# Kernel tuning notes

Measured on AMD Instinct MI355X. Metric: run time of the kernel, lower is better.

Reference implementation:

```python
import jax, jax.numpy as jnp
import numpy as np

B, S, F = 128, 256, 40
H, D, NH, L, FF = 64, 128, 4, 2, 2048
REG, BIN, NW = 8, 1, 3
NEG = -1e9


def _ln(x, s, b, eps=1e-5):
    m = x.mean(-1, keepdims=True)
    v = ((x - m) ** 2).mean(-1, keepdims=True)
    return (x - m) / jnp.sqrt(v + eps) * s + b


def setup_inputs() -> dict:
    key = jax.random.key(0)
    ks = list(jax.random.split(key, 40))
    k = iter(ks)
    def rn(shape, s=0.05):
        return jax.random.normal(next(k), shape, jnp.float32) * s
    inp = {}
    inp['x'] = jax.random.normal(next(k), (B, S, F), jnp.float32)
    inp['mask'] = jnp.ones((B, S, F), jnp.float32)
    inp['delta'] = jax.random.uniform(next(k), (B, S, F), jnp.float32)
    # GRU params (torch layout: [3H, in], gates order r,z,n)
    inp['gru_w_ih'] = rn((3 * H, 3 * F))
    inp['gru_w_hh'] = rn((3 * H, H))
    inp['gru_b_ih'] = rn((3 * H,))
    inp['gru_b_hh'] = rn((3 * H,))
    inp['dm_w'] = rn((D, H)); inp['dm_b'] = rn((D,))
    # transformer layers stacked on leading dim L
    inp['in_proj_w'] = rn((L, 3 * D, D)); inp['in_proj_b'] = rn((L, 3 * D))
    inp['out_proj_w'] = rn((L, D, D)); inp['out_proj_b'] = rn((L, D))
    inp['lin1_w'] = rn((L, FF, D)); inp['lin1_b'] = rn((L, FF))
    inp['lin2_w'] = rn((L, D, FF)); inp['lin2_b'] = rn((L, D))
    inp['ln1_s'] = jnp.ones((L, D), jnp.float32); inp['ln1_b'] = jnp.zeros((L, D), jnp.float32)
    inp['ln2_s'] = jnp.ones((L, D), jnp.float32); inp['ln2_b'] = jnp.zeros((L, D), jnp.float32)
    inp['score_w'] = rn((1, D)); inp['score_b'] = rn((1,))
    inp['reg_w'] = rn((NW, REG, D)); inp['reg_b'] = rn((NW, REG))
    inp['bin_w'] = rn((NW, BIN, D)); inp['bin_b'] = rn((NW, BIN))
    inp['window_id'] = jax.random.randint(next(k), (B,), 0, NW, jnp.int32)
    return inp


def reference(x, mask, delta, gru_w_ih, gru_w_hh, gru_b_ih, gru_b_hh, dm_w, dm_b,
              in_proj_w, in_proj_b, out_proj_w, out_proj_b, lin1_w, lin1_b,
              lin2_w, lin2_b, ln1_s, ln1_b, ln2_s, ln2_b, score_w, score_b,
              reg_w, reg_b, bin_w, bin_b, window_id):
    inp = jnp.concatenate([x, mask, delta], -1)          # [B,S,3F]
    xw = inp @ gru_w_ih.T + gru_b_ih                      # [B,S,3H] precomputed input gates

    def step(h, xw_t):
        gh = h @ gru_w_hh.T + gru_b_hh
        xr, xz, xn = jnp.split(xw_t, 3, -1)
        hr, hz, hn = jnp.split(gh, 3, -1)
        r = jax.nn.sigmoid(xr + hr)
        zg = jax.nn.sigmoid(xz + hz)
        n = jnp.tanh(xn + r * hn)
        h_new = (1.0 - zg) * n + zg * h
        return h_new, h_new

    h0 = jnp.zeros((x.shape[0], H), x.dtype)
    _, hs = jax.lax.scan(step, h0, jnp.swapaxes(xw, 0, 1))  # [S,B,H]
    z = jnp.swapaxes(hs, 0, 1) @ dm_w.T + dm_b              # [B,S,D]

    time_mask = mask.sum(-1) > 0                            # [B,S] bool
    bias = jnp.where(time_mask[:, None, None, :], 0.0, NEG).astype(z.dtype)
    dh = D // NH
    scale = 1.0 / np.sqrt(dh)

    for l in range(L):  # post-LN torch TransformerEncoderLayer
        qkv = z @ in_proj_w[l].T + in_proj_b[l]
        q, k, v = jnp.split(qkv, 3, -1)
        q = q.reshape(B, S, NH, dh).transpose(0, 2, 1, 3)
        k = k.reshape(B, S, NH, dh).transpose(0, 2, 1, 3)
        v = v.reshape(B, S, NH, dh).transpose(0, 2, 1, 3)
        attn = jax.nn.softmax(jnp.einsum('bhqd,bhkd->bhqk', q, k) * scale + bias, -1)
        o = jnp.einsum('bhqk,bhkd->bhqd', attn, v).transpose(0, 2, 1, 3).reshape(B, S, D)
        z = _ln(z + (o @ out_proj_w[l].T + out_proj_b[l]), ln1_s[l], ln1_b[l])
        ff = jax.nn.relu(z @ lin1_w[l].T + lin1_b[l]) @ lin2_w[l].T + lin2_b[l]
        z = _ln(z + ff, ln2_s[l], ln2_b[l])

    scores = (z @ score_w.T + score_b)[..., 0]              # [B,S]
    scores = jnp.where(time_mask, scores, NEG)
    alpha = jax.nn.softmax(scores, 1)
    pooled = jnp.einsum('bsd,bs->bd', z, alpha)             # [B,D]

    # routed heads: gather 1-of-3 head weights per sample, batched matvec
    y_reg = jnp.einsum('bod,bd->bo', reg_w[window_id], pooled) + reg_b[window_id]
    y_bin = jnp.einsum('bod,bd->bo', bin_w[window_id], pooled) + bin_b[window_id]
    return (y_reg, y_bin)
```

## Files before the change

kernel.cpp:

```cpp
#include <hip/hip_runtime.h>

typedef __attribute__((ext_vector_type(8))) short short8;
typedef __attribute__((ext_vector_type(4))) float f32x4;
typedef unsigned short u16;

#define BB   128
#define SS   256
#define FIN  40
#define HH   64
#define DD   128
#define NHH  4
#define LL   2
#define NEGV (-1e9f)

__device__ __forceinline__ u16 f2b(float f) {
    unsigned u = __float_as_uint(f);
    return (u16)((u + 0x7FFFu + ((u >> 16) & 1u)) >> 16);
}
__device__ __forceinline__ float b2f(u16 u) {
    return __uint_as_float(((unsigned)u) << 16);
}

__global__ __launch_bounds__(256) void cvt_all_kernel(const float* __restrict__ dm_w,
                                                      const float* __restrict__ ip_w,
                                                      const float* __restrict__ op_w,
                                                      const float* __restrict__ l1_w,
                                                      const float* __restrict__ l2_w,
                                                      u16* __restrict__ o_dm, u16* __restrict__ o_ip,
                                                      u16* __restrict__ o_op, u16* __restrict__ o_l1,
                                                      u16* __restrict__ o_l2) {
    int blk = blockIdx.x;
    const float* s; u16* d; int off;
    if      (blk < 4)   { s = dm_w; d = o_dm; off = blk; }
    else if (blk < 52)  { s = ip_w; d = o_ip; off = blk - 4; }
    else if (blk < 68)  { s = op_w; d = o_op; off = blk - 52; }
    else if (blk < 324) { s = l1_w; d = o_l1; off = blk - 68; }
    else                { s = l2_w; d = o_l2; off = blk - 324; }
    int i = (off * 256 + threadIdx.x) * 8;
    float4 a = *(const float4*)&s[i];
    float4 b = *(const float4*)&s[i + 4];
    short8 o;
    o[0] = (short)f2b(a.x); o[1] = (short)f2b(a.y); o[2] = (short)f2b(a.z); o[3] = (short)f2b(a.w);
    o[4] = (short)f2b(b.x); o[5] = (short)f2b(b.y); o[6] = (short)f2b(b.z); o[7] = (short)f2b(b.w);
    *(short8*)&d[i] = o;
}

__global__ __launch_bounds__(256) void tm_kernel(const float* __restrict__ mask,
                                                 float* __restrict__ tm) {
    int i = blockIdx.x * blockDim.x + threadIdx.x;
    if (i >= BB * SS) return;
    const float* m = mask + (size_t)i * FIN;
    float s = 0.f;
    for (int f = 0; f < FIN; ++f) s += m[f];
    tm[i] = (s > 0.f) ? 1.f : 0.f;
}

__global__ __launch_bounds__(192) void xw_kernel(const float* __restrict__ x,
                                                 const float* __restrict__ mask,
                                                 const float* __restrict__ delta,
                                                 const float* __restrict__ w_ih,
                                                 const float* __restrict__ b_ih,
                                                 float* __restrict__ xwt) {
    __shared__ float inp[16][120];
    __shared__ float wl[192][21];
    int group = blockIdx.x >> 8;
    int t = blockIdx.x & 255;
    int tid = threadIdx.x;

    for (int idx = tid; idx < 16 * 120; idx += 192) {
        int r = idx / 120, k = idx % 120;
        size_t g = (size_t)(group * 16 + r) * 256 + t;
        float v;
        if (k < 40)      v = x[g * FIN + k];
        else if (k < 80) v = mask[g * FIN + (k - 40)];
        else             v = delta[g * FIN + (k - 80)];
        inp[r][k] = v;
    }

    float acc[16];
#pragma unroll
    for (int r = 0; r < 16; ++r) acc[r] = 0.f;

    for (int kt = 0; kt < 6; ++kt) {
        __syncthreads();
        for (int idx = tid; idx < 192 * 20; idx += 192) {
            int r = idx / 20, k = idx % 20;
            wl[r][k] = w_ih[(size_t)r * 120 + kt * 20 + k];
        }
        __syncthreads();
#pragma unroll
        for (int kk = 0; kk < 20; ++kk) {
            float w = wl[tid][kk];
            int kg = kt * 20 + kk;
#pragma unroll
            for (int r = 0; r < 16; ++r) acc[r] += w * inp[r][kg];
        }
    }
    float bias = b_ih[tid];
    float* o = xwt + ((size_t)(group * 256 + t) * 192 + tid) * 16;
#pragma unroll
    for (int r = 0; r < 16; r += 4) {
        float4 v = {acc[r] + bias, acc[r + 1] + bias, acc[r + 2] + bias, acc[r + 3] + bias};
        *(float4*)&o[r] = v;
    }
}

__device__ __forceinline__ float gru_gate(float xr, float xz, float xn,
                                          float ar, float az, float an, float hold) {
    float r  = 1.f / (1.f + __expf(-(xr + ar)));
    float zg = 1.f / (1.f + __expf(-(xz + az)));
    float nx = xn + r * an;
    float n  = 2.f / (1.f + __expf(-2.f * nx)) - 1.f;
    return (1.f - zg) * n + zg * hold;
}

__global__ __launch_bounds__(512, 1) void gru_scan_kernel(const float* __restrict__ w_hh,
                                                          const float* __restrict__ b_hh,
                                                          const float* __restrict__ xwt,
                                                          u16* __restrict__ hsb) {
    __shared__ __align__(16) u16 hb[2][16 * 64];
    __shared__ __align__(16) u16 hstage[8][16 * 64];
    int b0 = blockIdx.x * 16;
    int tid = threadIdx.x;
    int w = tid >> 6, lane = tid & 63;
    int fr = lane & 15, hi = lane >> 4;
    int cw = w & 3;
    int jg = w >> 2;

    for (int idx = tid; idx < 1024; idx += 512) hb[0][idx] = 0;

    int c = cw * 16 + fr;
    float br_ = b_hh[c], bz_ = b_hh[64 + c], bn_ = b_hh[128 + c];

    short8 wfr[2], wfz[2], wfn[2];
#pragma unroll
    for (int ks = 0; ks < 2; ++ks) {
        int slot = ks * 4 + hi;
        const float* p0 = w_hh + (size_t)c * 64 + slot * 8;
        const float* p1 = w_hh + (size_t)(64 + c) * 64 + slot * 8;
        const float* p2 = w_hh + (size_t)(128 + c) * 64 + slot * 8;
#pragma unroll
        for (int q = 0; q < 8; ++q) {
            wfr[ks][q] = (short)f2b(p0[q]);
            wfz[ks][q] = (short)f2b(p1[q]);
            wfn[ks][q] = (short)f2b(p2[q]);
        }
    }

    const float* xg = xwt + (size_t)blockIdx.x * (256 * 192 * 16);
    int lo = hi * 4 + jg * 2;

    float hrA = 0.f, hrB = 0.f;

    int woA = (lo + 0) * 64 + ((((c >> 3) ^ ((lo + 0) & 7))) << 3) + (c & 7);
    int woB = (lo + 1) * 64 + ((((c >> 3) ^ ((lo + 1) & 7))) << 3) + (c & 7);
    int soA = (lo + 0) * 64 + c;
    int soB = (lo + 1) * 64 + c;

    float2 pxr[4], pxz[4], pxn[4];
#pragma unroll
    for (int u = 0; u < 4; ++u) {
        pxr[u] = *(const float2*)&xg[((size_t)u * 192 + c) * 16 + lo];
        pxz[u] = *(const float2*)&xg[((size_t)u * 192 + 64 + c) * 16 + lo];
        pxn[u] = *(const float2*)&xg[((size_t)u * 192 + 128 + c) * 16 + lo];
    }
    __syncthreads();

    int cur = 0;
    auto step = [&](float2 xr2, float2 xz2, float2 xn2, int ts) {
        f32x4 ar = {br_, br_, br_, br_};
        f32x4 az = {bz_, bz_, bz_, bz_};
        f32x4 an = {bn_, bn_, bn_, bn_};
#pragma unroll
        for (int ks = 0; ks < 2; ++ks) {
            int soff = (((ks << 2) + hi) ^ (fr & 7)) << 3;
            short8 af = *(const short8*)&hb[cur][fr * 64 + soff];
            ar = __builtin_amdgcn_mfma_f32_16x16x32_bf16(af, wfr[ks], ar, 0, 0, 0);
            az = __builtin_amdgcn_mfma_f32_16x16x32_bf16(af, wfz[ks], az, 0, 0, 0);
            an = __builtin_amdgcn_mfma_f32_16x16x32_bf16(af, wfn[ks], an, 0, 0, 0);
        }
        float aR0, aR1, aZ0, aZ1, aN0, aN1;
        if (jg == 0) { aR0 = ar[0]; aR1 = ar[1]; aZ0 = az[0]; aZ1 = az[1]; aN0 = an[0]; aN1 = an[1]; }
        else         { aR0 = ar[2]; aR1 = ar[3]; aZ0 = az[2]; aZ1 = az[3]; aN0 = an[2]; aN1 = an[3]; }
        hrA = gru_gate(xr2.x, xz2.x, xn2.x, aR0, aZ0, aN0, hrA);
        hrB = gru_gate(xr2.y, xz2.y, xn2.y, aR1, aZ1, aN1, hrB);
        u16 v0 = f2b(hrA), v1 = f2b(hrB);
        int nxt = cur ^ 1;
        hb[nxt][woA] = v0; hb[nxt][woB] = v1;
        hstage[ts][soA] = v0; hstage[ts][soB] = v1;
        asm volatile("s_waitcnt lgkmcnt(0)\n\ts_barrier" ::: "memory");
        cur = nxt;
    };

    for (int t = 0; t < SS; t += 8) {
#pragma unroll
        for (int u = 0; u < 8; ++u) {
            int tp = t + u + 4; tp = (tp < SS) ? tp : (SS - 1);
            float2 nr = *(const float2*)&xg[((size_t)tp * 192 + c) * 16 + lo];
            float2 nz = *(const float2*)&xg[((size_t)tp * 192 + 64 + c) * 16 + lo];
            float2 nn = *(const float2*)&xg[((size_t)tp * 192 + 128 + c) * 16 + lo];
            step(pxr[u & 3], pxz[u & 3], pxn[u & 3], u);
            pxr[u & 3] = nr; pxz[u & 3] = nz; pxn[u & 3] = nn;
        }
#pragma unroll
        for (int f = 0; f < 2; ++f) {
            int idx = tid + f * 512;
            int c8 = idx & 7, pair = idx >> 3;
            int ts = pair >> 4, row = pair & 15;
            short8 v = *(const short8*)&hstage[ts][row * 64 + c8 * 8];
            *(short8*)&hsb[((size_t)(b0 + row) * SS + t + ts) * 64 + c8 * 8] = v;
        }
        asm volatile("s_waitcnt lgkmcnt(0)\n\ts_barrier" ::: "memory");
    }
}

__device__ __forceinline__ void gl_lds16(const void* g, void* s) {
    __builtin_amdgcn_global_load_lds(
        (const __attribute__((address_space(1))) void*)g,
        (__attribute__((address_space(3))) void*)s, 16, 0, 0);
}

template <int MODE, bool RELU>
__global__ __launch_bounds__(256, 2) void mfma_gemm(const u16* __restrict__ A,
                                                    const u16* __restrict__ W,
                                                    const float* __restrict__ bias,
                                                    float* __restrict__ C,
                                                    u16* __restrict__ Cb,
                                                    const float* __restrict__ lns,
                                                    const float* __restrict__ lnb,
                                                    int M, int N, int K) {
    __shared__ __align__(16) u16 Al[128 * 64];
    __shared__ __align__(16) u16 Bl[128 * 64];
    __shared__ float lred[2][2][128];
    int bm = blockIdx.x, bn = blockIdx.y;
    int tid = threadIdx.x;
    int w = tid >> 6, lane = tid & 63;
    int wrow = (w >> 1) * 64, wcol = (w & 1) * 64;
    int fr = lane & 15, hi = lane >> 4;
    int rl = lane >> 3;
    int sl = lane & 7;
    int ssl = sl ^ rl;

    const u16* Ag = A + ((size_t)bm * 128) * K + ssl * 8;
    const u16* Wg = W + ((size_t)bn * 128) * K + ssl * 8;

    f32x4 acc[4][4];
#pragma unroll
    for (int i = 0; i < 4; ++i)
#pragma unroll
        for (int jj = 0; jj < 4; ++jj) acc[i][jj] = (f32x4){0.f, 0.f, 0.f, 0.f};

    int ar[4], br[4];
#pragma unroll
    for (int m = 0; m < 4; ++m) {
        ar[m] = (wrow + m * 16 + fr) * 64;
        br[m] = (wcol + m * 16 + fr) * 64;
    }
    int swz = (fr & 7);

    for (int kt = 0; kt < K; kt += 64) {
        __syncthreads();
#pragma unroll
        for (int i = 0; i < 4; ++i) {
            int c = w * 4 + i;
            int row = c * 8 + rl;
            gl_lds16(Ag + (size_t)row * K + kt, &Al[c * 512]);
            gl_lds16(Wg + (size_t)row * K + kt, &Bl[c * 512]);
        }
        __syncthreads();
#pragma unroll
        for (int kk = 0; kk < 2; ++kk) {
            short8 a[4], bq[4];
            int soff = (((kk << 2) + hi) ^ swz) << 3;
#pragma unroll
            for (int m = 0; m < 4; ++m)
                a[m] = *(const short8*)&Al[ar[m] + soff];
#pragma unroll
            for (int n = 0; n < 4; ++n)
                bq[n] = *(const short8*)&Bl[br[n] + soff];
#pragma unroll
            for (int m = 0; m < 4; ++m)
#pragma unroll
                for (int n = 0; n < 4; ++n)
                    acc[m][n] = __builtin_amdgcn_mfma_f32_16x16x32_bf16(a[m], bq[n], acc[m][n], 0, 0, 0);
        }
    }

    float bv[4];
#pragma unroll
    for (int n = 0; n < 4; ++n) bv[n] = bias[bn * 128 + wcol + n * 16 + fr];

    if (MODE == 4) {
        float v[4][4][4];
#pragma unroll
        for (int m = 0; m < 4; ++m)
#pragma unroll
            for (int j = 0; j < 4; ++j) {
                int row = bm * 128 + wrow + m * 16 + hi * 4 + j;
#pragma unroll
                for (int n = 0; n < 4; ++n)
                    v[m][n][j] = acc[m][n][j] + bv[n] + C[(size_t)row * 128 + wcol + n * 16 + fr];
            }
#pragma unroll
        for (int m = 0; m < 4; ++m)
#pragma unroll
            for (int j = 0; j < 4; ++j) {
                float s = v[m][0][j] + v[m][1][j] + v[m][2][j] + v[m][3][j];
                float q = v[m][0][j]*v[m][0][j] + v[m][1][j]*v[m][1][j]
                        + v[m][2][j]*v[m][2][j] + v[m][3][j]*v[m][3][j];
#pragma unroll
                for (int off = 1; off <= 8; off <<= 1) {
                    s += __shfl_xor(s, off);
                    q += __shfl_xor(q, off);
                }
                if (fr == 0) {
                    int lrow = wrow + m * 16 + hi * 4 + j;
                    lred[0][w & 1][lrow] = s;
                    lred[1][w & 1][lrow] = q;
                }
            }
        __syncthreads();
        float sv[4], bb[4];
#pragma unroll
        for (int n = 0; n < 4; ++n) {
            sv[n] = lns[wcol + n * 16 + fr];
            bb[n] = lnb[wcol + n * 16 + fr];
        }
#pragma unroll
        for (int m = 0; m < 4; ++m)
#pragma unroll
            for (int j = 0; j < 4; ++j) {
                int lrow = wrow + m * 16 + hi * 4 + j;
                float mean = (lred[0][0][lrow] + lred[0][1][lrow]) * (1.f / 128.f);
                float msq  = (lred[1][0][lrow] + lred[1][1][lrow]) * (1.f / 128.f);
                float rstd = rsqrtf(msq - mean * mean + 1e-5f);
                int row = bm * 128 + lrow;
#pragma unroll
                for (int n = 0; n < 4; ++n) {
                    int col = wcol + n * 16 + fr;
                    float o = (v[m][n][j] - mean) * rstd * sv[n] + bb[n];
                    C[(size_t)row * 128 + col] = o;
                    Cb[(size_t)row * 128 + col] = f2b(o);
                }
            }
    } else {
#pragma unroll
        for (int m = 0; m < 4; ++m) {
#pragma unroll
            for (int j = 0; j < 4; ++j) {
                int row = bm * 128 + wrow + m * 16 + hi * 4 + j;
#pragma unroll
                for (int n = 0; n < 4; ++n) {
                    int col = bn * 128 + wcol + n * 16 + fr;
                    float vv = acc[m][n][j] + bv[n];
                    if (RELU) vv = fmaxf(vv, 0.f);
                    if (MODE & 1) C[(size_t)row * N + col] = vv;
                    if (MODE & 2) Cb[(size_t)row * N + col] = f2b(vv);
                }
            }
        }
    }
}

__global__ __launch_bounds__(256, 1) void ff_fused_kernel(const u16* __restrict__ zbin,
                                                          const u16* __restrict__ w1,
                                                          const float* __restrict__ b1,
                                                          const u16* __restrict__ w2,
                                                          const float* __restrict__ b2,
                                                          const float* __restrict__ lns,
                                                          const float* __restrict__ lnb,
                                                          float* __restrict__ z,
                                                          u16* __restrict__ zbout) {
    __shared__ __align__(16) u16 ZB[2][128 * 64];
    __shared__ __align__(16) u16 W1C[2][128 * 64];
    __shared__ __align__(16) u16 W2C[2][128 * 64];
    __shared__ __align__(16) u16 A1[2][128 * 64];
    __shared__ float lred[2][2][128];
    int bm = blockIdx.x;
    int tid = threadIdx.x;
    int w = tid >> 6, lane = tid & 63;
    int wrow = (w >> 1) * 64, wcol = (w & 1) * 64;
    int fr = lane & 15, hi = lane >> 4;
    int rl = lane >> 3, ssl = (lane & 7) ^ rl;
    int swz = fr & 7;
    int xh = wrow >> 6;

#pragma unroll
    for (int hk = 0; hk < 2; ++hk)
#pragma unroll
        for (int i = 0; i < 4; ++i) {
            int ch = w * 4 + i, row = ch * 8 + rl;
            gl_lds16(zbin + ((size_t)(bm * 128 + row)) * 128 + hk * 64 + ssl * 8, &ZB[hk][ch * 512]);
        }

    f32x4 acc2[4][4];
#pragma unroll
    for (int m = 0; m < 4; ++m)
#pragma unroll
        for (int n = 0; n < 4; ++n) acc2[m][n] = (f32x4){0.f, 0.f, 0.f, 0.f};

    for (int ci = 0; ci < 16; ++ci) {
#pragma unroll
        for (int hk = 0; hk < 2; ++hk)
#pragma unroll
            for (int i = 0; i < 4; ++i) {
                int ch = w * 4 + i, row = ch * 8 + rl;
                gl_lds16(w1 + ((size_t)(ci * 128 + row)) * 128 + hk * 64 + ssl * 8, &W1C[hk][ch * 512]);
                gl_lds16(w2 + ((size_t)row) * 2048 + ci * 128 + hk * 64 + ssl * 8, &W2C[hk][ch * 512]);
            }
        __syncthreads();

        f32x4 acc1[4][4];
#pragma unroll
        for (int m = 0; m < 4; ++m)
#pragma unroll
            for (int n = 0; n < 4; ++n) acc1[m][n] = (f32x4){0.f, 0.f, 0.f, 0.f};
#pragma unroll
        for (int ks = 0; ks < 4; ++ks) {
            int hk = ks >> 1;
            int soff = ((((ks & 1) << 2) + hi) ^ swz) << 3;
            short8 a[4], b[4];
#pragma unroll
            for (int m = 0; m < 4; ++m)
                a[m] = *(const short8*)&W1C[hk][(wrow + m * 16 + fr) * 64 + soff];
#pragma unroll
            for (int n = 0; n < 4; ++n)
                b[n] = *(const short8*)&ZB[hk][(wcol + n * 16 + fr) * 64 + soff];
#pragma unroll
            for (int m = 0; m < 4; ++m)
#pragma unroll
                for (int n = 0; n < 4; ++n)
                    acc1[m][n] = __builtin_amdgcn_mfma_f32_16x16x32_bf16(a[m], b[n], acc1[m][n], 0, 0, 0);
        }
#pragma unroll
        for (int m = 0; m < 4; ++m) {
            int x0 = wrow + m * 16 + hi * 4;
            float4 bb = *(const float4*)&b1[ci * 128 + x0];
            int slot = (x0 & 63) >> 3;
            int wadd = x0 & 7;
#pragma unroll
            for (int n = 0; n < 4; ++n) {
                int r = wcol + n * 16 + fr;
                float v0 = fmaxf(acc1[m][n][0] + bb.x, 0.f);
                float v1 = fmaxf(acc1[m][n][1] + bb.y, 0.f);
                float v2 = fmaxf(acc1[m][n][2] + bb.z, 0.f);
                float v3 = fmaxf(acc1[m][n][3] + bb.w, 0.f);
                uint2 pk;
                pk.x = (unsigned)f2b(v0) | ((unsigned)f2b(v1) << 16);
                pk.y = (unsigned)f2b(v2) | ((unsigned)f2b(v3) << 16);
                *(uint2*)&A1[xh][r * 64 + ((slot ^ (r & 7)) << 3) + wadd] = pk;
            }
        }
        __syncthreads();

#pragma unroll
        for (int ks = 0; ks < 4; ++ks) {
            int hk = ks >> 1;
            int soff = ((((ks & 1) << 2) + hi) ^ swz) << 3;
            short8 a[4], b[4];
#pragma unroll
            for (int m = 0; m < 4; ++m)
                a[m] = *(const short8*)&W2C[hk][(wrow + m * 16 + fr) * 64 + soff];
#pragma unroll
            for (int n = 0; n < 4; ++n)
                b[n] = *(const short8*)&A1[hk][(wcol + n * 16 + fr) * 64 + soff];
#pragma unroll
            for (int m = 0; m < 4; ++m)
#pragma unroll
                for (int n = 0; n < 4; ++n)
                    acc2[m][n] = __builtin_amdgcn_mfma_f32_16x16x32_bf16(a[m], b[n], acc2[m][n], 0, 0, 0);
        }
        __syncthreads();
    }

    float vv[4][4][4];
#pragma unroll
    for (int m = 0; m < 4; ++m) {
        int x0 = wrow + m * 16 + hi * 4;
        float4 bb = *(const float4*)&b2[x0];
#pragma unroll
        for (int n = 0; n < 4; ++n) {
            int y = wcol + n * 16 + fr;
            float4 zo = *(const float4*)&z[((size_t)(bm * 128 + y)) * 128 + x0];
            vv[m][n][0] = acc2[m][n][0] + bb.x + zo.x;
            vv[m][n][1] = acc2[m][n][1] + bb.y + zo.y;
            vv[m][n][2] = acc2[m][n][2] + bb.z + zo.z;
            vv[m][n][3] = acc2[m][n][3] + bb.w + zo.w;
        }
    }
#pragma unroll
    for (int n = 0; n < 4; ++n) {
        float s = 0.f, q = 0.f;
#pragma unroll
        for (int m = 0; m < 4; ++m)
#pragma unroll
            for (int j = 0; j < 4; ++j) { float v = vv[m][n][j]; s += v; q += v * v; }
        s += __shfl_xor(s, 16); s += __shfl_xor(s, 32);
        q += __shfl_xor(q, 16); q += __shfl_xor(q, 32);
        if (hi == 0) {
            int y = wcol + n * 16 + fr;
            lred[0][xh][y] = s;
            lred[1][xh][y] = q;
        }
    }
    __syncthreads();
#pragma unroll
    for (int n = 0; n < 4; ++n) {
        int y = wcol + n * 16 + fr;
        float mean = (lred[0][0][y] + lred[0][1][y]) * (1.f / 128.f);
        float msq  = (lred[1][0][y] + lred[1][1][y]) * (1.f / 128.f);
        float rstd = rsqrtf(msq - mean * mean + 1e-5f);
#pragma unroll
        for (int m = 0; m < 4; ++m) {
            int x0 = wrow + m * 16 + hi * 4;
            float4 sv = *(const float4*)&lns[x0];
            float4 bv = *(const float4*)&lnb[x0];
            float o0 = (vv[m][n][0] - mean) * rstd * sv.x + bv.x;
            float o1 = (vv[m][n][1] - mean) * rstd * sv.y + bv.y;
            float o2 = (vv[m][n][2] - mean) * rstd * sv.z + bv.z;
            float o3 = (vv[m][n][3] - mean) * rstd * sv.w + bv.w;
            size_t zoff = ((size_t)(bm * 128 + y)) * 128 + x0;
            *(float4*)&z[zoff] = (float4){o0, o1, o2, o3};
            uint2 pk;
            pk.x = (unsigned)f2b(o0) | ((unsigned)f2b(o1) << 16);
            pk.y = (unsigned)f2b(o2) | ((unsigned)f2b(o3) << 16);
            *(uint2*)&zbout[zoff] = pk;
        }
    }
}

__global__ __launch_bounds__(256) void attn_mfma_kernel(const u16* __restrict__ qkv,
                                                        const float* __restrict__ tm,
                                                        u16* __restrict__ attno) {
    __shared__ __align__(16) u16 Kl[256 * 40];
    __shared__ __align__(16) u16 Vt[32 * 264];
    __shared__ __align__(16) u16 Pl[4][64 * 72];
    __shared__ float tmb[256];
    int bh = blockIdx.x;
    int b = bh >> 2, hd = bh & 3;
    int tid = threadIdx.x;
    int w = tid >> 6, lane = tid & 63;
    int fr = lane & 15, hi = lane >> 4;
    const u16* base = qkv + (size_t)b * SS * 384 + hd * 32;

    for (int idx = tid; idx < 1024; idx += 256) {
        int r = idx >> 2, s = idx & 3;
        short8 v = *(const short8*)(base + (size_t)r * 384 + 128 + s * 8);
        *(short8*)&Kl[r * 40 + s * 8] = v;
    }
    for (int idx = tid; idx < 1024; idx += 256) {
        int r = idx >> 2, s = idx & 3;
        short8 v = *(const short8*)(base + (size_t)r * 384 + 256 + s * 8);
#pragma unroll
        for (int q = 0; q < 8; ++q) Vt[(s * 8 + q) * 264 + r] = (u16)v[q];
    }
    tmb[tid] = (tm[b * SS + tid] > 0.f) ? 0.f : NEGV;

    int q0 = w * 64;
    short8 qf[4];
#pragma unroll
    for (int m = 0; m < 4; ++m)
        qf[m] = *(const short8*)(base + (size_t)(q0 + m * 16 + fr) * 384 + hi * 8);
    __syncthreads();

    const float scale = 0.17677669529663687f;
    f32x4 accO[4][2];
#pragma unroll
    for (int m = 0; m < 4; ++m) {
        accO[m][0] = (f32x4){0.f, 0.f, 0.f, 0.f};
        accO[m][1] = (f32x4){0.f, 0.f, 0.f, 0.f};
    }
    float den[4][4];
#pragma unroll
    for (int m = 0; m < 4; ++m)
#pragma unroll
        for (int j = 0; j < 4; ++j) den[m][j] = 0.f;

    u16* pw = &Pl[w][0];

    for (int kt = 0; kt < 4; ++kt) {
        f32x4 accS[4][4];
#pragma unroll
        for (int m = 0; m < 4; ++m)
#pragma unroll
            for (int n = 0; n < 4; ++n) accS[m][n] = (f32x4){0.f, 0.f, 0.f, 0.f};
        short8 kf[4];
#pragma unroll
        for (int n = 0; n < 4; ++n)
            kf[n] = *(const short8*)&Kl[(kt * 64 + n * 16 + fr) * 40 + hi * 8];
#pragma unroll
        for (int m = 0; m < 4; ++m)
#pragma unroll
            for (int n = 0; n < 4; ++n)
                accS[m][n] = __builtin_amdgcn_mfma_f32_16x16x32_bf16(qf[m], kf[n], accS[m][n], 0, 0, 0);

        float bias[4];
#pragma unroll
        for (int n = 0; n < 4; ++n) bias[n] = tmb[kt * 64 + n * 16 + fr];

#pragma unroll
        for (int m = 0; m < 4; ++m) {
            float rs0 = 0.f, rs1 = 0.f, rs2 = 0.f, rs3 = 0.f;
#pragma unroll
            for (int n = 0; n < 4; ++n) {
                float p0 = __expf(accS[m][n][0] * scale + bias[n]);
                float p1 = __expf(accS[m][n][1] * scale + bias[n]);
                float p2 = __expf(accS[m][n][2] * scale + bias[n]);
                float p3 = __expf(accS[m][n][3] * scale + bias[n]);
                rs0 += p0; rs1 += p1; rs2 += p2; rs3 += p3;
                int cb = n * 16 + fr;
                pw[(m * 16 + hi * 4 + 0) * 72 + cb] = f2b(p0);
                pw[(m * 16 + hi * 4 + 1) * 72 + cb] = f2b(p1);
                pw[(m * 16 + hi * 4 + 2) * 72 + cb] = f2b(p2);
                pw[(m * 16 + hi * 4 + 3) * 72 + cb] = f2b(p3);
            }
#pragma unroll
            for (int off = 1; off <= 8; off <<= 1) {
                rs0 += __shfl_xor(rs0, off);
                rs1 += __shfl_xor(rs1, off);
                rs2 += __shfl_xor(rs2, off);
                rs3 += __shfl_xor(rs3, off);
            }
            den[m][0] += rs0; den[m][1] += rs1; den[m][2] += rs2; den[m][3] += rs3;
        }
        asm volatile("s_waitcnt lgkmcnt(0)" ::: "memory");

#pragma unroll
        for (int ks = 0; ks < 2; ++ks) {
            short8 pf[4], vf[2];
#pragma unroll
            for (int m = 0; m < 4; ++m)
                pf[m] = *(const short8*)&pw[(m * 16 + fr) * 72 + ks * 32 + hi * 8];
#pragma unroll
            for (int nd = 0; nd < 2; ++nd)
                vf[nd] = *(const short8*)&Vt[(nd * 16 + fr) * 264 + kt * 64 + ks * 32 + hi * 8];
#pragma unroll
            for (int m = 0; m < 4; ++m)
#pragma unroll
                for (int nd = 0; nd < 2; ++nd)
                    accO[m][nd] = __builtin_amdgcn_mfma_f32_16x16x32_bf16(pf[m], vf[nd], accO[m][nd], 0, 0, 0);
        }
    }

    u16* orow = attno + (size_t)(b * SS + q0) * DD + hd * 32;
#pragma unroll
    for (int m = 0; m < 4; ++m)
#pragma unroll
        for (int j = 0; j < 4; ++j) {
            float inv = 1.f / den[m][j];
            int qr = m * 16 + hi * 4 + j;
            orow[(size_t)qr * DD + fr]      = f2b(accO[m][0][j] * inv);
            orow[(size_t)qr * DD + 16 + fr] = f2b(accO[m][1][j] * inv);
        }
}

__global__ __launch_bounds__(256) void pool_all_kernel(const float* __restrict__ z,
                                                       const float* __restrict__ score_w,
                                                       const float* __restrict__ score_b,
                                                       const float* __restrict__ tm,
                                                       const float* __restrict__ reg_w,
                                                       const float* __restrict__ reg_b,
                                                       const float* __restrict__ bin_w,
                                                       const float* __restrict__ bin_b,
                                                       const int* __restrict__ wid,
                                                       float* __restrict__ out) {
    int b = blockIdx.x;
    int tid = threadIdx.x;
    __shared__ float sw[128];
    __shared__ float al[SS];
    __shared__ float red[8];
    __shared__ float pp[2][128];
    __shared__ float p[128];

    if (tid < 128) sw[tid] = score_w[tid];
    __syncthreads();

    const float* zr = z + ((size_t)b * SS + tid) * DD;
    float acc = 0.f;
#pragma unroll
    for (int j = 0; j < 128; j += 4) {
        float4 a = *(const float4*)&zr[j];
        float4 wv = *(const float4*)&sw[j];
        acc += a.x * wv.x + a.y * wv.y + a.z * wv.z + a.w * wv.w;
    }
    float sc = acc + score_b[0];
    sc = (tm[b * SS + tid] > 0.f) ? sc : NEGV;

    float m = sc;
#pragma unroll
    for (int off = 32; off; off >>= 1) m = fmaxf(m, __shfl_xor(m, off));
    if ((tid & 63) == 0) red[tid >> 6] = m;
    __syncthreads();
    m = fmaxf(fmaxf(red[0], red[1]), fmaxf(red[2], red[3]));
    float e = __expf(sc - m);
    float ssum = e;
#pragma unroll
    for (int off = 32; off; off >>= 1) ssum += __shfl_xor(ssum, off);
    if ((tid & 63) == 0) red[4 + (tid >> 6)] = ssum;
    __syncthreads();
    ssum = red[4] + red[5] + red[6] + red[7];
    al[tid] = e / ssum;
    __syncthreads();

    int d = tid & 127, half = tid >> 7;
    float pa = 0.f;
    for (int t = half; t < SS; t += 2) pa += al[t] * z[((size_t)b * SS + t) * DD + d];
    pp[half][d] = pa;
    __syncthreads();
    if (tid < 128) p[tid] = pp[0][tid] + pp[1][tid];
    __syncthreads();

    if (tid < 9) {
        int wi = wid[b];
        const float* wrow;
        float bias;
        if (tid < 8) { wrow = reg_w + ((size_t)wi * 8 + tid) * 128; bias = reg_b[wi * 8 + tid]; }
        else         { wrow = bin_w + (size_t)wi * 128;             bias = bin_b[wi]; }
        float hacc = bias;
        for (int k = 0; k < 128; ++k) hacc += wrow[k] * p[k];
        if (tid < 8) out[b * 8 + tid] = hacc;
        else         out[1024 + b] = hacc;
    }
}

extern "C" void kernel_launch(void* const* d_in, const int* in_sizes, int n_in,
                              void* d_out, int out_size, void* d_ws, size_t ws_size,
                              hipStream_t stream) {
    const float* x         = (const float*)d_in[0];
    const float* mask      = (const float*)d_in[1];
    const float* delta     = (const float*)d_in[2];
    const float* gru_w_ih  = (const float*)d_in[3];
    const float* gru_w_hh  = (const float*)d_in[4];
    const float* gru_b_ih  = (const float*)d_in[5];
    const float* gru_b_hh  = (const float*)d_in[6];
    const float* dm_w      = (const float*)d_in[7];
    const float* dm_b      = (const float*)d_in[8];
    const float* in_proj_w = (const float*)d_in[9];
    const float* in_proj_b = (const float*)d_in[10];
    const float* out_proj_w= (const float*)d_in[11];
    const float* out_proj_b= (const float*)d_in[12];
    const float* lin1_w    = (const float*)d_in[13];
    const float* lin1_b    = (const float*)d_in[14];
    const float* lin2_w    = (const float*)d_in[15];
    const float* lin2_b    = (const float*)d_in[16];
    const float* ln1_s     = (const float*)d_in[17];
    const float* ln1_bb    = (const float*)d_in[18];
    const float* ln2_s     = (const float*)d_in[19];
    const float* ln2_bb    = (const float*)d_in[20];
    const float* score_w   = (const float*)d_in[21];
    const float* score_b   = (const float*)d_in[22];
    const float* reg_w     = (const float*)d_in[23];
    const float* reg_b     = (const float*)d_in[24];
    const float* bin_w     = (const float*)d_in[25];
    const float* bin_b     = (const float*)d_in[26];
    const int*   window_id = (const int*)d_in[27];
    float* out = (float*)d_out;

    char* w8 = (char*)d_ws;
    float* z      = (float*)(w8 + 0);
    u16*   zb     = (u16*)  (w8 + 16777216);
    u16*   hsb    = (u16*)  (w8 + 25165824);
    u16*   wb_dm  = (u16*)  (w8 + 29360128);
    u16*   wb_ip  = (u16*)  (w8 + 29376512);
    u16*   wb_op  = (u16*)  (w8 + 29573120);
    u16*   wb_l1  = (u16*)  (w8 + 29638656);
    u16*   wb_l2  = (u16*)  (w8 + 30687232);
    float* tm     = (float*)(w8 + 31735808);
    float* xwt    = (float*)(w8 + 32063488);
    u16*   qkvb   = (u16*)  (w8 + 32063488);
    u16*   attnob = (u16*)  (w8 + 57229312);

    cvt_all_kernel<<<580, 256, 0, stream>>>(dm_w, in_proj_w, out_proj_w, lin1_w, lin2_w,
                                            wb_dm, wb_ip, wb_op, wb_l1, wb_l2);

    tm_kernel<<<(BB * SS + 255) / 256, 256, 0, stream>>>(mask, tm);
    xw_kernel<<<2048, 192, 0, stream>>>(x, mask, delta, gru_w_ih, gru_b_ih, xwt);
    gru_scan_kernel<<<8, 512, 0, stream>>>(gru_w_hh, gru_b_hh, xwt, hsb);

    mfma_gemm<3, false><<<dim3(256, 1), 256, 0, stream>>>(
        hsb, wb_dm, dm_b, z, zb, nullptr, nullptr, 32768, 128, 64);

    for (int l = 0; l < LL; ++l) {
        mfma_gemm<2, false><<<dim3(256, 3), 256, 0, stream>>>(
            zb, wb_ip + (size_t)l * 49152, in_proj_b + l * 384, nullptr, qkvb,
            nullptr, nullptr, 32768, 384, 128);
        attn_mfma_kernel<<<BB * NHH, 256, 0, stream>>>(qkvb, tm, attnob);
        mfma_gemm<4, false><<<dim3(256, 1), 256, 0, stream>>>(
            attnob, wb_op + (size_t)l * 16384, out_proj_b + l * 128, z, zb,
            ln1_s + l * 128, ln1_bb + l * 128, 32768, 128, 128);
        ff_fused_kernel<<<256, 256, 0, stream>>>(
            zb, wb_l1 + (size_t)l * 262144, lin1_b + l * 2048,
            wb_l2 + (size_t)l * 262144, lin2_b + l * 128,
            ln2_s + l * 128, ln2_bb + l * 128, z, zb);
    }

    pool_all_kernel<<<BB, 256, 0, stream>>>(z, score_w, score_b, tm,
                                            reg_w, reg_b, bin_w, bin_b, window_id, out);
}
```

Baseline: 503.0 us.

## Stage GRU input gates into LDS via async double-buffered global_load_lds

```diff
diff --git a/kernel.cpp b/kernel.cpp
--- a/kernel.cpp
+++ b/kernel.cpp
@@ -19,6 +19,12 @@
 }
 __device__ __forceinline__ float b2f(u16 u) {
     return __uint_as_float(((unsigned)u) << 16);
+}
+
+__device__ __forceinline__ void gl_lds16(const void* g, void* s) {
+    __builtin_amdgcn_global_load_lds(
+        (const __attribute__((address_space(1))) void*)g,
+        (__attribute__((address_space(3))) void*)s, 16, 0, 0);
 }
 
 __global__ __launch_bounds__(256) void cvt_all_kernel(const float* __restrict__ dm_w,
@@ -118,8 +124,9 @@
                                                           const float* __restrict__ b_hh,
                                                           const float* __restrict__ xwt,
                                                           u16* __restrict__ hsb) {
+    __shared__ __align__(16) float xbuf[2][4 * 3072];
     __shared__ __align__(16) u16 hb[2][16 * 64];
-    __shared__ __align__(16) u16 hstage[8][16 * 64];
+    __shared__ __align__(16) u16 hstage[4][16 * 64];
     int b0 = blockIdx.x * 16;
     int tid = threadIdx.x;
     int w = tid >> 6, lane = tid & 63;
@@ -147,7 +154,7 @@
         }
     }
 
-    const float* xg = xwt + (size_t)blockIdx.x * (256 * 192 * 16);
+    const char* xgb = (const char*)(xwt + (size_t)blockIdx.x * (256 * 192 * 16));
     int lo = hi * 4 + jg * 2;
 
     float hrA = 0.f, hrB = 0.f;
@@ -157,67 +164,61 @@
     int soA = (lo + 0) * 64 + c;
     int soB = (lo + 1) * 64 + c;
 
-    float2 pxr[4], pxz[4], pxn[4];
-#pragma unroll
-    for (int u = 0; u < 4; ++u) {
-        pxr[u] = *(const float2*)&xg[((size_t)u * 192 + c) * 16 + lo];
-        pxz[u] = *(const float2*)&xg[((size_t)u * 192 + 64 + c) * 16 + lo];
-        pxn[u] = *(const float2*)&xg[((size_t)u * 192 + 128 + c) * 16 + lo];
-    }
+    auto stage = [&](int g, int buf) {
+#pragma unroll
+        for (int i = 0; i < 6; ++i) {
+            int ch = w * 6 + i;
+            gl_lds16(xgb + (size_t)g * 49152 + ch * 1024 + lane * 16,
+                     (char*)&xbuf[buf][0] + ch * 1024 + lane * 16);
+        }
+    };
+
+    stage(0, 0);
+    asm volatile("s_waitcnt vmcnt(0)" ::: "memory");
     __syncthreads();
 
-    int cur = 0;
-    auto step = [&](float2 xr2, float2 xz2, float2 xn2, int ts) {
-        f32x4 ar = {br_, br_, br_, br_};
-        f32x4 az = {bz_, bz_, bz_, bz_};
-        f32x4 an = {bn_, bn_, bn_, bn_};
-#pragma unroll
-        for (int ks = 0; ks < 2; ++ks) {
-            int soff = (((ks << 2) + hi) ^ (fr & 7)) << 3;
-            short8 af = *(const short8*)&hb[cur][fr * 64 + soff];
-            ar = __builtin_amdgcn_mfma_f32_16x16x32_bf16(af, wfr[ks], ar, 0, 0, 0);
-            az = __builtin_amdgcn_mfma_f32_16x16x32_bf16(af, wfz[ks], az, 0, 0, 0);
-            an = __builtin_amdgcn_mfma_f32_16x16x32_bf16(af, wfn[ks], an, 0, 0, 0);
-        }
-        float aR0, aR1, aZ0, aZ1, aN0, aN1;
-        if (jg == 0) { aR0 = ar[0]; aR1 = ar[1]; aZ0 = az[0]; aZ1 = az[1]; aN0 = an[0]; aN1 = an[1]; }
-        else         { aR0 = ar[2]; aR1 = ar[3]; aZ0 = az[2]; aZ1 = az[3]; aN0 = an[2]; aN1 = an[3]; }
-        hrA = gru_gate(xr2.x, xz2.x, xn2.x, aR0, aZ0, aN0, hrA);
-        hrB = gru_gate(xr2.y, xz2.y, xn2.y, aR1, aZ1, aN1, hrB);
-        u16 v0 = f2b(hrA), v1 = f2b(hrB);
-        int nxt = cur ^ 1;
-        hb[nxt][woA] = v0; hb[nxt][woB] = v1;
-        hstage[ts][soA] = v0; hstage[ts][soB] = v1;
-        asm volatile("s_waitcnt lgkmcnt(0)\n\ts_barrier" ::: "memory");
-        cur = nxt;
-    };
-
-    for (int t = 0; t < SS; t += 8) {
-#pragma unroll
-        for (int u = 0; u < 8; ++u) {
-            int tp = t + u + 4; tp = (tp < SS) ? tp : (SS - 1);
-            float2 nr = *(const float2*)&xg[((size_t)tp * 192 + c) * 16 + lo];
-            float2 nz = *(const float2*)&xg[((size_t)tp * 192 + 64 + c) * 16 + lo];
-            float2 nn = *(const float2*)&xg[((size_t)tp * 192 + 128 + c) * 16 + lo];
-            step(pxr[u & 3], pxz[u & 3], pxn[u & 3], u);
-            pxr[u & 3] = nr; pxz[u & 3] = nz; pxn[u & 3] = nn;
-        }
-#pragma unroll
-        for (int f = 0; f < 2; ++f) {
-            int idx = tid + f * 512;
-            int c8 = idx & 7, pair = idx >> 3;
+    int cur = 0, buf = 0;
+    for (int g = 0; g < 64; ++g) {
+        if (g + 1 < 64) stage(g + 1, buf ^ 1);
+#pragma unroll
+        for (int ts = 0; ts < 4; ++ts) {
+            const float* xs = &xbuf[buf][ts * 3072];
+            float2 xr2 = *(const float2*)&xs[c * 16 + lo];
+            float2 xz2 = *(const float2*)&xs[(64 + c) * 16 + lo];
+            float2 xn2 = *(const float2*)&xs[(128 + c) * 16 + lo];
+
+            f32x4 ar = {br_, br_, br_, br_};
+            f32x4 az = {bz_, bz_, bz_, bz_};
+            f32x4 an = {bn_, bn_, bn_, bn_};
+#pragma unroll
+            for (int ks = 0; ks < 2; ++ks) {
+                int soff = (((ks << 2) + hi) ^ (fr & 7)) << 3;
+                short8 af = *(const short8*)&hb[cur][fr * 64 + soff];
+                ar = __builtin_amdgcn_mfma_f32_16x16x32_bf16(af, wfr[ks], ar, 0, 0, 0);
+                az = __builtin_amdgcn_mfma_f32_16x16x32_bf16(af, wfz[ks], az, 0, 0, 0);
+                an = __builtin_amdgcn_mfma_f32_16x16x32_bf16(af, wfn[ks], an, 0, 0, 0);
+            }
+            float aR0, aR1, aZ0, aZ1, aN0, aN1;
+            if (jg == 0) { aR0 = ar[0]; aR1 = ar[1]; aZ0 = az[0]; aZ1 = az[1]; aN0 = an[0]; aN1 = an[1]; }
+            else         { aR0 = ar[2]; aR1 = ar[3]; aZ0 = az[2]; aZ1 = az[3]; aN0 = an[2]; aN1 = an[3]; }
+            hrA = gru_gate(xr2.x, xz2.x, xn2.x, aR0, aZ0, aN0, hrA);
+            hrB = gru_gate(xr2.y, xz2.y, xn2.y, aR1, aZ1, aN1, hrB);
+            u16 v0 = f2b(hrA), v1 = f2b(hrB);
+            int nxt = cur ^ 1;
+            hb[nxt][woA] = v0; hb[nxt][woB] = v1;
+            hstage[ts][soA] = v0; hstage[ts][soB] = v1;
+            asm volatile("s_waitcnt lgkmcnt(0)\n\ts_barrier" ::: "memory");
+            cur = nxt;
+        }
+        {
+            int c8 = tid & 7, pair = tid >> 3;
             int ts = pair >> 4, row = pair & 15;
             short8 v = *(const short8*)&hstage[ts][row * 64 + c8 * 8];
-            *(short8*)&hsb[((size_t)(b0 + row) * SS + t + ts) * 64 + c8 * 8] = v;
-        }
-        asm volatile("s_waitcnt lgkmcnt(0)\n\ts_barrier" ::: "memory");
-    }
-}
-
-__device__ __forceinline__ void gl_lds16(const void* g, void* s) {
-    __builtin_amdgcn_global_load_lds(
-        (const __attribute__((address_space(1))) void*)g,
-        (__attribute__((address_space(3))) void*)s, 16, 0, 0);
+            *(short8*)&hsb[((size_t)(b0 + row) * SS + g * 4 + ts) * 64 + c8 * 8] = v;
+        }
+        asm volatile("s_waitcnt vmcnt(1) lgkmcnt(0)\n\ts_barrier" ::: "memory");
+        buf ^= 1;
+    }
 }
 
 template <int MODE, bool RELU>
```

Result: slower. 535.5 us (+6.5%).
